# Optimization experiments

Measured on AMD Instinct MI355X. Metric: run time of the kernel, lower is better.

The kernel has to match this reference:

```python
import jax, jax.numpy as jnp
import numpy as np

CONF_THRES = 0.25
IOU_THRES = 0.45
MAX_DET = 1000
MAX_WH = 4096.0   # class offset for per-class NMS (yolov5 trick)
TOPK = 2048       # pre-NMS candidate cap (fixed-shape stand-in for max_nms)


def _xywh2xyxy(b):
    cx, cy, w, h = b[..., 0], b[..., 1], b[..., 2], b[..., 3]
    return jnp.stack([cx - w * 0.5, cy - h * 0.5, cx + w * 0.5, cy + h * 0.5], axis=-1)


def _box_iou(a, b):
    # a, b: [K, 4] in xyxy -> [K, K] pairwise IoU
    lt = jnp.maximum(a[:, None, :2], b[None, :, :2])
    rb = jnp.minimum(a[:, None, 2:], b[None, :, 2:])
    wh = jnp.clip(rb - lt, 0.0)
    inter = wh[..., 0] * wh[..., 1]
    area_a = (a[:, 2] - a[:, 0]) * (a[:, 3] - a[:, 1])
    area_b = (b[:, 2] - b[:, 0]) * (b[:, 3] - b[:, 1])
    return inter / (area_a[:, None] + area_b[None, :] - inter + 1e-7)


def _nms_single(pred):
    # pred: [N, 5+C] = (cx, cy, w, h, obj, cls...)
    obj = pred[:, 4]
    cls_prob = pred[:, 5:]
    cls_conf = jnp.max(cls_prob, axis=-1)
    cls_id = jnp.argmax(cls_prob, axis=-1)
    score = obj * cls_conf                      # conf = obj_conf * cls_conf (best class)
    valid = (obj > CONF_THRES) & (score > CONF_THRES)
    score = jnp.where(valid, score, 0.0)
    boxes = _xywh2xyxy(pred[:, :4])

    # keep top-K candidates by confidence (sorted descending)
    tops, idx = jax.lax.top_k(score, TOPK)
    boxes_k = boxes[idx]                        # [K, 4]
    cls_k = cls_id[idx]                         # [K]
    val_k = tops > 0.0

    # per-class NMS via class offset
    shifted = boxes_k + (cls_k.astype(boxes_k.dtype) * MAX_WH)[:, None]
    iou = _box_iou(shifted, shifted)            # [K, K]

    j = jnp.arange(TOPK)

    def body(i, keep):
        # if box i survives, suppress lower-scored boxes with IoU > thresh
        sup = keep[i] & (iou[i] > IOU_THRES) & (j > i)
        return keep & ~sup

    keep = jax.lax.fori_loop(0, TOPK, body, val_k)

    # gather up to MAX_DET kept detections (already score-sorted)
    fs, fi = jax.lax.top_k(jnp.where(keep, tops, -1.0), MAX_DET)
    ok = fs > 0.0
    det_boxes = jnp.where(ok[:, None], boxes_k[fi], 0.0)
    det_score = jnp.where(ok, tops[fi], 0.0)
    det_cls = jnp.where(ok, cls_k[fi].astype(det_boxes.dtype), -1.0)
    # [MAX_DET, 6] = (x1, y1, x2, y2, conf, cls); padded rows have conf 0, cls -1
    return jnp.concatenate([det_boxes, det_score[:, None], det_cls[:, None]], axis=-1)


def setup_inputs() -> dict:
    key = jax.random.key(0)
    raw = jax.random.uniform(key, (16, 25200, 85), dtype=jnp.float32)
    xy = raw[..., 0:2] * 640.0            # centers within a 640x640 image
    wh = raw[..., 2:4] * 120.0 + 2.0      # box sizes in [2, 122]
    rest = raw[..., 4:]                   # obj + class probs in [0, 1)
    pred = jnp.concatenate([xy, wh, rest], axis=-1)
    return {"pred": pred}


def reference(pred):
    return jax.vmap(_nms_single)(pred)
```

## Files before the change

### kernel.cpp

```cpp
#include <hip/hip_runtime.h>
#include <stdint.h>

#pragma clang fp contract(off)

#define BB 16
#define NN 25200
#define ROW 85
#define NCLS 80
#define TK 2048
#define SORTN 4096
#define NBIN 4096
#define MAXDET 1000
#define CONF 0.25f
#define IOUT 0.45f
#define SROWS 64
#define STH 0x3E800000u
#define MCAP 256

typedef float fvec4 __attribute__((ext_vector_type(4)));

#define AS1 __attribute__((address_space(1)))
#define AS3 __attribute__((address_space(3)))

__global__ __launch_bounds__(128) void score_kernel(const float* __restrict__ pred,
                                                    float* __restrict__ scores,
                                                    uint8_t* __restrict__ cls,
                                                    unsigned int* __restrict__ hist) {
  __shared__ __align__(16) float srow[SROWS * ROW];
  const int tile = blockIdx.x;
  const int b = blockIdx.y;
  const int tid = threadIdx.x;
  const int lane = tid & 63;
  const int row0 = tile * SROWS;
  int nrows = NN - row0;
  if (nrows > SROWS) nrows = SROWS;
  const char* gsrc = (const char*)(pred + ((size_t)b * NN + row0) * ROW);
  const int nbytes = nrows * ROW * 4;
  for (int off = tid * 16; off < nbytes; off += 128 * 16) {
    __builtin_amdgcn_global_load_lds((AS1 void*)(gsrc + off),
                                     (AS3 void*)((char*)srow + (off - lane * 16)),
                                     16, 0, 0);
  }
  __builtin_amdgcn_s_waitcnt(0);
  __syncthreads();
  if (tid < nrows) {
    const int n = row0 + tid;
    const float* r = srow + tid * ROW;
    float obj = r[4];
    float best = r[5];
    int bid = 0;
#pragma unroll
    for (int c = 1; c < NCLS; ++c) {
      float p = r[5 + c];
      if (p > best) { best = p; bid = c; }
    }
    float score = obj * best;
    bool valid = (obj > CONF) && (score > CONF);
    float sout = valid ? score : 0.0f;
    scores[(size_t)b * NN + n] = sout;
    cls[(size_t)b * NN + n] = (uint8_t)bid;
    if (valid) {
      unsigned int u = __float_as_uint(sout);
      unsigned int bin = (u - (STH + 1u)) >> 12;
      if (bin > NBIN - 1) bin = NBIN - 1;
      atomicAdd(&hist[(size_t)b * NBIN + bin], 1u);
    }
  }
}

__global__ __launch_bounds__(256) void scan_kernel(const unsigned int* __restrict__ hist,
                                                   unsigned int* __restrict__ gsoff,
                                                   int* __restrict__ gP,
                                                   int* __restrict__ gtot) {
  const int b = blockIdx.x;
  const int t = threadIdx.x;
  const int w = t >> 6, lane = t & 63;
  const unsigned int* h = hist + (size_t)b * NBIN;
  unsigned int loc[16];
  int ssum = 0;
#pragma unroll
  for (int k = 0; k < 16; ++k) {
    loc[k] = h[NBIN - 1 - (16 * t + k)];
    ssum += (int)loc[k];
  }
  int v = ssum;
  for (int o = 1; o < 64; o <<= 1) { int u = __shfl_up(v, o); if (lane >= o) v += u; }
  __shared__ int sw[4];
  __shared__ int sfound;
  if (t == 0) sfound = 0;
  if (lane == 63) sw[w] = v;
  __syncthreads();
  int wbase = 0;
  for (int i = 0; i < w; ++i) wbase += sw[i];
  const int total = sw[0] + sw[1] + sw[2] + sw[3];
  int run = wbase + v - ssum;
#pragma unroll
  for (int k = 0; k < 16; ++k) {
    int bin = NBIN - 1 - (16 * t + k);
    gsoff[(size_t)b * NBIN + bin] = (unsigned int)run;
    int c = (int)loc[k];
    if (run < TK && run + c >= TK) {
      gP[b] = bin;
      gtot[b] = run + c;
      sfound = 1;
    }
    run += c;
  }
  __syncthreads();
  if (t == 0 && !sfound) { gP[b] = 0; gtot[b] = total; }
}

__global__ __launch_bounds__(1024) void scatter_kernel(const float* __restrict__ scores,
                                                       const unsigned int* __restrict__ gsoff,
                                                       const int* __restrict__ gP,
                                                       unsigned int* __restrict__ gcnt,
                                                       unsigned long long* __restrict__ gskey) {
  const int b = blockIdx.y;
  const int n = blockIdx.x * 1024 + threadIdx.x;
  if (n >= NN) return;
  const unsigned int P = (unsigned int)gP[b];
  unsigned int u = __float_as_uint(scores[(size_t)b * NN + n]);
  if (u > STH) {
    unsigned int bin = (u - (STH + 1u)) >> 12;
    if (bin > NBIN - 1) bin = NBIN - 1;
    if (bin >= P) {
      unsigned int pos = gsoff[(size_t)b * NBIN + bin] +
                         atomicAdd(&gcnt[(size_t)b * NBIN + bin], 1u);
      if (pos < SORTN)
        gskey[(size_t)b * SORTN + pos] = ((unsigned long long)u << 32) | (unsigned int)(~n);
    }
  }
}

__global__ __launch_bounds__(1024) void emit_kernel(const float* __restrict__ pred,
                                                    const uint8_t* __restrict__ cls,
                                                    const unsigned int* __restrict__ gsoff,
                                                    const unsigned int* __restrict__ gcnt,
                                                    const unsigned long long* __restrict__ gskey,
                                                    const int* __restrict__ gtot,
                                                    float* __restrict__ gtops,
                                                    fvec4* __restrict__ gbox,
                                                    int* __restrict__ gcls) {
  const int b = blockIdx.y;
  const int stride = gridDim.x * 1024;
  const int tot = gtot[b];
  const int used = tot < SORTN ? tot : SORTN;
  const int npos = tot < TK ? tot : TK;
  for (int ip = npos + blockIdx.x * 1024 + threadIdx.x; ip < TK; ip += stride) {
    gtops[(size_t)b * TK + ip] = 0.0f;
    gcls[(size_t)b * TK + ip] = 0xFFFF;
    fvec4 z; z[0] = 0.f; z[1] = 0.f; z[2] = 0.f; z[3] = 0.f;
    gbox[(size_t)b * TK + ip] = z;
  }
  for (int pp = blockIdx.x * 1024 + threadIdx.x; pp < used; pp += stride) {
    unsigned long long k = gskey[(size_t)b * SORTN + pp];
    unsigned int u = (unsigned int)(k >> 32);
    unsigned int bin = (u - (STH + 1u)) >> 12;
    if (bin > NBIN - 1) bin = NBIN - 1;
    int base = (int)gsoff[(size_t)b * NBIN + bin];
    int cnt = (int)gcnt[(size_t)b * NBIN + bin];
    if (base + cnt > used) cnt = used - base;
    const unsigned long long* seg = gskey + (size_t)b * SORTN + base;
    int rank = 0;
    for (int j = 0; j < cnt; ++j) rank += (seg[j] > k) ? 1 : 0;
    int q = base + rank;
    if (q < npos) {
      int idx = (int)(~(unsigned int)k);
      gtops[(size_t)b * TK + q] = __uint_as_float(u);
      gcls[(size_t)b * TK + q] = (int)cls[(size_t)b * NN + idx];
      const float* rowp = pred + ((size_t)b * NN + idx) * ROW;
      float cx = rowp[0], cy = rowp[1], w2 = rowp[2], h2 = rowp[3];
      float hw = w2 * 0.5f, hh = h2 * 0.5f;
      fvec4 bb4;
      bb4[0] = cx - hw; bb4[1] = cy - hh; bb4[2] = cx + hw; bb4[3] = cy + hh;
      gbox[(size_t)b * TK + q] = bb4;
    }
  }
}

__global__ __launch_bounds__(64) void nms_kernel(const float* __restrict__ gtops,
                                                 const fvec4* __restrict__ gbox,
                                                 const int* __restrict__ gcls,
                                                 int* __restrict__ keep) {
  const int c = blockIdx.x;
  const int b = blockIdx.y;
  const int lane = threadIdx.x;
  __shared__ unsigned short spos[TK];
  __shared__ float mx1[MCAP], my1[MCAP], mx2[MCAP], my2[MCAP];
  __shared__ unsigned char skp[TK];

  int m = 0;
  for (int base = 0; base < TK; base += 64) {
    int j = base + lane;
    bool match = (gcls[(size_t)b * TK + j] == c);
    unsigned long long bal = __ballot(match);
    int mp = m + __popcll(bal & ((1ull << lane) - 1ull));
    if (match) {
      spos[mp] = (unsigned short)j;
      skp[mp] = (gtops[(size_t)b * TK + j] > 0.0f) ? 1 : 0;
      if (mp < MCAP) {
        fvec4 bx = gbox[(size_t)b * TK + j];
        mx1[mp] = bx[0]; my1[mp] = bx[1]; mx2[mp] = bx[2]; my2[mp] = bx[3];
      }
    }
    m += (int)__popcll(bal);
  }
  __syncthreads();

  float b0x1 = 0.f, b0y1 = 0.f, b0x2 = 0.f, b0y2 = 0.f;
  if (lane < m) { b0x1 = mx1[lane]; b0y1 = my1[lane]; b0x2 = mx2[lane]; b0y2 = my2[lane]; }
  __syncthreads();

  for (int i = 0; i < m; ++i) {
    if (!skp[i]) continue;
    float ax1, ay1, ax2, ay2;
    if (i < 64) {
      ax1 = __shfl(b0x1, i); ay1 = __shfl(b0y1, i);
      ax2 = __shfl(b0x2, i); ay2 = __shfl(b0y2, i);
    } else if (i < MCAP) {
      ax1 = mx1[i]; ay1 = my1[i]; ax2 = mx2[i]; ay2 = my2[i];
    } else {
      fvec4 bx = gbox[(size_t)b * TK + spos[i]];
      ax1 = bx[0]; ay1 = bx[1]; ax2 = bx[2]; ay2 = bx[3];
    }
    float aarea = (ax2 - ax1) * (ay2 - ay1);
    for (int q = 0; q * 64 < m; ++q) {
      int j = q * 64 + lane;
      if (j > i && j < m && skp[j]) {
        float jx1, jy1, jx2, jy2;
        if (q == 0) { jx1 = b0x1; jy1 = b0y1; jx2 = b0x2; jy2 = b0y2; }
        else if (j < MCAP) { jx1 = mx1[j]; jy1 = my1[j]; jx2 = mx2[j]; jy2 = my2[j]; }
        else { fvec4 bx = gbox[(size_t)b * TK + spos[j]];
               jx1 = bx[0]; jy1 = bx[1]; jx2 = bx[2]; jy2 = bx[3]; }
        float ltx = fmaxf(ax1, jx1), lty = fmaxf(ay1, jy1);
        float rbx = fminf(ax2, jx2), rby = fminf(ay2, jy2);
        float iw = fmaxf(rbx - ltx, 0.0f);
        float ih = fmaxf(rby - lty, 0.0f);
        float inter = iw * ih;
        float barea = (jx2 - jx1) * (jy2 - jy1);
        float iou = inter / (aarea + barea - inter + 1e-7f);
        if (iou > IOUT) skp[j] = 0;
      }
    }
  }
  __syncthreads();

  for (int i = lane; i < m; i += 64) {
    keep[(size_t)b * TK + spos[i]] = skp[i];
  }
}

__global__ __launch_bounds__(256) void out_kernel(const float* __restrict__ gtops,
                                                  const fvec4* __restrict__ gbox,
                                                  const int* __restrict__ gcls,
                                                  const int* __restrict__ keep,
                                                  const int* __restrict__ gtot,
                                                  float* __restrict__ out) {
  int b = blockIdx.x;
  int t = threadIdx.x;
  __shared__ int scnt[256];
  int npos = gtot[b];
  if (npos > TK) npos = TK;
  const int CH = TK / 256;
  int base = t * CH;
  int kp[CH];
  int cnt = 0;
  for (int k = 0; k < CH; ++k) {
    int j = base + k;
    kp[k] = (j < npos) ? keep[(size_t)b * TK + j] : 0;
    cnt += kp[k];
  }
  scnt[t] = cnt;
  __syncthreads();
  for (int off = 1; off < 256; off <<= 1) {
    int v = (t >= off) ? scnt[t - off] : 0;
    __syncthreads();
    scnt[t] += v;
    __syncthreads();
  }
  int r = scnt[t] - cnt;
  int K = scnt[255];
  for (int k = 0; k < CH; ++k) {
    if (kp[k]) {
      if (r < MAXDET) {
        int j = base + k;
        float* o = out + ((size_t)b * MAXDET + r) * 6;
        fvec4 bx = gbox[(size_t)b * TK + j];
        o[0] = bx[0]; o[1] = bx[1]; o[2] = bx[2]; o[3] = bx[3];
        o[4] = gtops[(size_t)b * TK + j];
        o[5] = (float)gcls[(size_t)b * TK + j];
      }
      ++r;
    }
  }
  int Kc = K < MAXDET ? K : MAXDET;
  for (int r2 = Kc + t; r2 < MAXDET; r2 += 256) {
    float* o = out + ((size_t)b * MAXDET + r2) * 6;
    o[0] = 0.0f; o[1] = 0.0f; o[2] = 0.0f; o[3] = 0.0f; o[4] = 0.0f; o[5] = -1.0f;
  }
}

extern "C" void kernel_launch(void* const* d_in, const int* in_sizes, int n_in,
                              void* d_out, int out_size, void* d_ws, size_t ws_size,
                              hipStream_t stream) {
  const float* pred = (const float*)d_in[0];
  float* out = (float*)d_out;

  char* ws = (char*)d_ws;
  size_t off = 0;
  float*              scores = (float*)(ws + off);              off += (size_t)BB * NN * 4;
  uint8_t*            cls    = (uint8_t*)(ws + off);            off += (size_t)BB * NN;
  off = (off + 255) & ~(size_t)255;
  unsigned int*       hist   = (unsigned int*)(ws + off);       off += (size_t)BB * NBIN * 4;
  unsigned int*       gcnt   = (unsigned int*)(ws + off);       off += (size_t)BB * NBIN * 4;
  unsigned int*       gsoff  = (unsigned int*)(ws + off);       off += (size_t)BB * NBIN * 4;
  unsigned long long* gskey  = (unsigned long long*)(ws + off); off += (size_t)BB * SORTN * 8;
  float*              gtops  = (float*)(ws + off);              off += (size_t)BB * TK * 4;
  fvec4*              gbox   = (fvec4*)(ws + off);              off += (size_t)BB * TK * 16;
  int*                gcls   = (int*)(ws + off);                off += (size_t)BB * TK * 4;
  int*                keep   = (int*)(ws + off);                off += (size_t)BB * TK * 4;
  int*                gP     = (int*)(ws + off);                off += (size_t)BB * 4;
  int*                gtot   = (int*)(ws + off);                off += (size_t)BB * 4;
  (void)ws_size; (void)in_sizes; (void)n_in; (void)out_size;

  hipMemsetAsync(hist, 0, (size_t)BB * NBIN * 4 * 2, stream);
  score_kernel<<<dim3((NN + SROWS - 1) / SROWS, BB), 128, 0, stream>>>(pred, scores, cls, hist);
  scan_kernel<<<BB, 256, 0, stream>>>(hist, gsoff, gP, gtot);
  scatter_kernel<<<dim3((NN + 1023) / 1024, BB), 1024, 0, stream>>>(scores, gsoff, gP, gcnt, gskey);
  emit_kernel<<<dim3(SORTN / 1024, BB), 1024, 0, stream>>>(pred, cls, gsoff, gcnt, gskey, gtot,
                                                           gtops, gbox, gcls);
  nms_kernel<<<dim3(NCLS, BB), 64, 0, stream>>>(gtops, gbox, gcls, keep);
  out_kernel<<<BB, 256, 0, stream>>>(gtops, gbox, gcls, keep, gtot, out);
}
```

Before: 247.3 us.

## Fold histogram scan into scatter and emit kernels, drop scan launch

Removes the separate scan kernel. Each scatter and emit block now recomputes the 4096-bin suffix scan of the histogram in shared memory. This removes one launch and the global round trip for offsets and threshold bin, at the cost of redundant scan work in every block. The emit kernel also zeroes keep for padding slots, so out_kernel can drop its bounds check and use a wave-shuffle scan instead of a shared-memory Hillis-Steele scan.

```diff
diff --git a/kernel.cpp b/kernel.cpp
--- a/kernel.cpp
+++ b/kernel.cpp
@@ -68,64 +68,62 @@
   }
 }
 
-__global__ __launch_bounds__(256) void scan_kernel(const unsigned int* __restrict__ hist,
-                                                   unsigned int* __restrict__ gsoff,
-                                                   int* __restrict__ gP,
-                                                   int* __restrict__ gtot) {
-  const int b = blockIdx.x;
-  const int t = threadIdx.x;
-  const int w = t >> 6, lane = t & 63;
-  const unsigned int* h = hist + (size_t)b * NBIN;
-  unsigned int loc[16];
+__device__ __forceinline__ void suffix_scan_1024(const unsigned int* __restrict__ h,
+                                                 unsigned int* soff, int* swsum,
+                                                 int* sPP, int* sTT,
+                                                 int t, int w, int lane) {
+  int loc[4];
   int ssum = 0;
 #pragma unroll
-  for (int k = 0; k < 16; ++k) {
-    loc[k] = h[NBIN - 1 - (16 * t + k)];
-    ssum += (int)loc[k];
+  for (int k = 0; k < 4; ++k) {
+    loc[k] = (int)h[NBIN - 1 - (4 * t + k)];
+    ssum += loc[k];
   }
   int v = ssum;
-  for (int o = 1; o < 64; o <<= 1) { int u = __shfl_up(v, o); if (lane >= o) v += u; }
-  __shared__ int sw[4];
-  __shared__ int sfound;
-  if (t == 0) sfound = 0;
-  if (lane == 63) sw[w] = v;
-  __syncthreads();
-  int wbase = 0;
-  for (int i = 0; i < w; ++i) wbase += sw[i];
-  const int total = sw[0] + sw[1] + sw[2] + sw[3];
-  int run = wbase + v - ssum;
+  for (int o = 1; o < 64; o <<= 1) { int uu = __shfl_up(v, o); if (lane >= o) v += uu; }
+  if (lane == 63) swsum[w] = v;
+  if (t == 0) *sPP = -1;
+  __syncthreads();
+  if (w == 0) {
+    int x = (lane < 16) ? swsum[lane] : 0;
+    for (int o = 1; o < 16; o <<= 1) { int uu = __shfl_up(x, o); if (lane >= o) x += uu; }
+    if (lane < 16) swsum[lane] = x;
+  }
+  __syncthreads();
+  const int total = swsum[15];
+  int run = (w ? swsum[w - 1] : 0) + (v - ssum);
 #pragma unroll
-  for (int k = 0; k < 16; ++k) {
-    int bin = NBIN - 1 - (16 * t + k);
-    gsoff[(size_t)b * NBIN + bin] = (unsigned int)run;
-    int c = (int)loc[k];
-    if (run < TK && run + c >= TK) {
-      gP[b] = bin;
-      gtot[b] = run + c;
-      sfound = 1;
-    }
-    run += c;
-  }
-  __syncthreads();
-  if (t == 0 && !sfound) { gP[b] = 0; gtot[b] = total; }
+  for (int k = 0; k < 4; ++k) {
+    int bin = NBIN - 1 - (4 * t + k);
+    soff[bin] = (unsigned int)run;
+    if (run < TK && run + loc[k] >= TK) { *sPP = bin; *sTT = run + loc[k]; }
+    run += loc[k];
+  }
+  __syncthreads();
+  if (t == 0 && *sPP < 0) { *sPP = 0; *sTT = total; }
+  __syncthreads();
 }
 
 __global__ __launch_bounds__(1024) void scatter_kernel(const float* __restrict__ scores,
-                                                       const unsigned int* __restrict__ gsoff,
-                                                       const int* __restrict__ gP,
+                                                       const unsigned int* __restrict__ hist,
                                                        unsigned int* __restrict__ gcnt,
                                                        unsigned long long* __restrict__ gskey) {
   const int b = blockIdx.y;
-  const int n = blockIdx.x * 1024 + threadIdx.x;
+  const int t = threadIdx.x;
+  const int w = t >> 6, lane = t & 63;
+  __shared__ unsigned int soff[NBIN];
+  __shared__ int swsum[16];
+  __shared__ int sP, sT;
+  suffix_scan_1024(hist + (size_t)b * NBIN, soff, swsum, &sP, &sT, t, w, lane);
+  const int P = sP;
+  const int n = blockIdx.x * 1024 + t;
   if (n >= NN) return;
-  const unsigned int P = (unsigned int)gP[b];
   unsigned int u = __float_as_uint(scores[(size_t)b * NN + n]);
   if (u > STH) {
     unsigned int bin = (u - (STH + 1u)) >> 12;
     if (bin > NBIN - 1) bin = NBIN - 1;
-    if (bin >= P) {
-      unsigned int pos = gsoff[(size_t)b * NBIN + bin] +
-                         atomicAdd(&gcnt[(size_t)b * NBIN + bin], 1u);
+    if ((int)bin >= P) {
+      unsigned int pos = soff[bin] + atomicAdd(&gcnt[(size_t)b * NBIN + bin], 1u);
       if (pos < SORTN)
         gskey[(size_t)b * SORTN + pos] = ((unsigned long long)u << 32) | (unsigned int)(~n);
     }
@@ -134,31 +132,39 @@
 
 __global__ __launch_bounds__(1024) void emit_kernel(const float* __restrict__ pred,
                                                     const uint8_t* __restrict__ cls,
-                                                    const unsigned int* __restrict__ gsoff,
-                                                    const unsigned int* __restrict__ gcnt,
+                                                    const unsigned int* __restrict__ hist,
                                                     const unsigned long long* __restrict__ gskey,
-                                                    const int* __restrict__ gtot,
                                                     float* __restrict__ gtops,
                                                     fvec4* __restrict__ gbox,
-                                                    int* __restrict__ gcls) {
+                                                    int* __restrict__ gcls,
+                                                    int* __restrict__ keep) {
   const int b = blockIdx.y;
-  const int stride = gridDim.x * 1024;
-  const int tot = gtot[b];
+  const int t = threadIdx.x;
+  const int w = t >> 6, lane = t & 63;
+  __shared__ unsigned int soff[NBIN];
+  __shared__ int swsum[16];
+  __shared__ int sP, sT;
+  const unsigned int* h = hist + (size_t)b * NBIN;
+  suffix_scan_1024(h, soff, swsum, &sP, &sT, t, w, lane);
+  const int tot = sT;
   const int used = tot < SORTN ? tot : SORTN;
   const int npos = tot < TK ? tot : TK;
-  for (int ip = npos + blockIdx.x * 1024 + threadIdx.x; ip < TK; ip += stride) {
+  const int pp = blockIdx.x * 1024 + t;
+  int ip = npos + pp;
+  if (ip < TK) {
     gtops[(size_t)b * TK + ip] = 0.0f;
     gcls[(size_t)b * TK + ip] = 0xFFFF;
+    keep[(size_t)b * TK + ip] = 0;
     fvec4 z; z[0] = 0.f; z[1] = 0.f; z[2] = 0.f; z[3] = 0.f;
     gbox[(size_t)b * TK + ip] = z;
   }
-  for (int pp = blockIdx.x * 1024 + threadIdx.x; pp < used; pp += stride) {
+  if (pp < used) {
     unsigned long long k = gskey[(size_t)b * SORTN + pp];
     unsigned int u = (unsigned int)(k >> 32);
     unsigned int bin = (u - (STH + 1u)) >> 12;
     if (bin > NBIN - 1) bin = NBIN - 1;
-    int base = (int)gsoff[(size_t)b * NBIN + bin];
-    int cnt = (int)gcnt[(size_t)b * NBIN + bin];
+    int base = (int)soff[bin];
+    int cnt = (int)h[bin];
     if (base + cnt > used) cnt = used - base;
     const unsigned long long* seg = gskey + (size_t)b * SORTN + base;
     int rank = 0;
@@ -190,6 +196,7 @@
   __shared__ unsigned char skp[TK];
 
   int m = 0;
+#pragma unroll 4
   for (int base = 0; base < TK; base += 64) {
     int j = base + lane;
     bool match = (gcls[(size_t)b * TK + j] == c);
@@ -254,32 +261,27 @@
                                                   const fvec4* __restrict__ gbox,
                                                   const int* __restrict__ gcls,
                                                   const int* __restrict__ keep,
-                                                  const int* __restrict__ gtot,
                                                   float* __restrict__ out) {
   int b = blockIdx.x;
   int t = threadIdx.x;
-  __shared__ int scnt[256];
-  int npos = gtot[b];
-  if (npos > TK) npos = TK;
+  int w = t >> 6, lane = t & 63;
+  __shared__ int sw4[4];
   const int CH = TK / 256;
   int base = t * CH;
   int kp[CH];
   int cnt = 0;
   for (int k = 0; k < CH; ++k) {
-    int j = base + k;
-    kp[k] = (j < npos) ? keep[(size_t)b * TK + j] : 0;
+    kp[k] = keep[(size_t)b * TK + base + k];
     cnt += kp[k];
   }
-  scnt[t] = cnt;
-  __syncthreads();
-  for (int off = 1; off < 256; off <<= 1) {
-    int v = (t >= off) ? scnt[t - off] : 0;
-    __syncthreads();
-    scnt[t] += v;
-    __syncthreads();
-  }
-  int r = scnt[t] - cnt;
-  int K = scnt[255];
+  int v = cnt;
+  for (int o = 1; o < 64; o <<= 1) { int u = __shfl_up(v, o); if (lane >= o) v += u; }
+  if (lane == 63) sw4[w] = v;
+  __syncthreads();
+  int wbase = 0;
+  for (int i = 0; i < w; ++i) wbase += sw4[i];
+  int K = sw4[0] + sw4[1] + sw4[2] + sw4[3];
+  int r = wbase + v - cnt;
   for (int k = 0; k < CH; ++k) {
     if (kp[k]) {
       if (r < MAXDET) {
@@ -313,22 +315,18 @@
   off = (off + 255) & ~(size_t)255;
   unsigned int*       hist   = (unsigned int*)(ws + off);       off += (size_t)BB * NBIN * 4;
   unsigned int*       gcnt   = (unsigned int*)(ws + off);       off += (size_t)BB * NBIN * 4;
-  unsigned int*       gsoff  = (unsigned int*)(ws + off);       off += (size_t)BB * NBIN * 4;
   unsigned long long* gskey  = (unsigned long long*)(ws + off); off += (size_t)BB * SORTN * 8;
   float*              gtops  = (float*)(ws + off);              off += (size_t)BB * TK * 4;
   fvec4*              gbox   = (fvec4*)(ws + off);              off += (size_t)BB * TK * 16;
   int*                gcls   = (int*)(ws + off);                off += (size_t)BB * TK * 4;
   int*                keep   = (int*)(ws + off);                off += (size_t)BB * TK * 4;
-  int*                gP     = (int*)(ws + off);                off += (size_t)BB * 4;
-  int*                gtot   = (int*)(ws + off);                off += (size_t)BB * 4;
   (void)ws_size; (void)in_sizes; (void)n_in; (void)out_size;
 
   hipMemsetAsync(hist, 0, (size_t)BB * NBIN * 4 * 2, stream);
   score_kernel<<<dim3((NN + SROWS - 1) / SROWS, BB), 128, 0, stream>>>(pred, scores, cls, hist);
-  scan_kernel<<<BB, 256, 0, stream>>>(hist, gsoff, gP, gtot);
-  scatter_kernel<<<dim3((NN + 1023) / 1024, BB), 1024, 0, stream>>>(scores, gsoff, gP, gcnt, gskey);
-  emit_kernel<<<dim3(SORTN / 1024, BB), 1024, 0, stream>>>(pred, cls, gsoff, gcnt, gskey, gtot,
-                                                           gtops, gbox, gcls);
+  scatter_kernel<<<dim3((NN + 1023) / 1024, BB), 1024, 0, stream>>>(scores, hist, gcnt, gskey);
+  emit_kernel<<<dim3(SORTN / 1024, BB), 1024, 0, stream>>>(pred, cls, hist, gskey,
+                                                           gtops, gbox, gcls, keep);
   nms_kernel<<<dim3(NCLS, BB), 64, 0, stream>>>(gtops, gbox, gcls, keep);
-  out_kernel<<<BB, 256, 0, stream>>>(gtops, gbox, gcls, keep, gtot, out);
-}
+  out_kernel<<<BB, 256, 0, stream>>>(gtops, gbox, gcls, keep, out);
+}
```

After: 244.4 us (median of 2 runs). Within noise of the previous version (-1.2%).
